# Performance work log

Measured on AMD Instinct MI355X. Metric: run time of the kernel, lower is better.

The kernel has to match this reference:

```python
import jax, jax.numpy as jnp
import numpy as np

EPS = 1e-5  # 'eps' forward arg, fixed as in typical transformer LayerNorm


def setup_inputs() -> dict:
    key = jax.random.key(0)
    ks = jax.random.split(key, 9)
    B, S, D = 4, 2048, 2048
    scale = 0.02
    return {
        "inputs": jax.random.normal(ks[0], (B, S, D), jnp.float32),
        "norm_weight": jax.random.uniform(ks[1], (D,), jnp.float32),
        "norm_bias": jax.random.normal(ks[2], (D,), jnp.float32) * scale,
        "q_weight": jax.random.normal(ks[3], (D, D), jnp.float32) * scale,
        "q_bias": jax.random.normal(ks[4], (D,), jnp.float32) * scale,
        "k_weight": jax.random.normal(ks[5], (D, D), jnp.float32) * scale,
        "k_bias": jax.random.normal(ks[6], (D,), jnp.float32) * scale,
        "v_weight": jax.random.normal(ks[7], (D, D), jnp.float32) * scale,
        "v_bias": jax.random.normal(ks[8], (D,), jnp.float32) * scale,
        "trans_b": 1,
        "shape_param": 0,
    }


def _layernorm(x, w, b, eps):
    mu = jnp.mean(x, axis=-1, keepdims=True)
    var = jnp.mean(jnp.square(x - mu), axis=-1, keepdims=True)
    return (x - mu) * jax.lax.rsqrt(var + eps) * w + b


def reference(inputs, norm_weight, norm_bias, q_weight, q_bias,
              k_weight, k_bias, v_weight, v_bias, trans_b, shape_param):
    # fused LayerNorm + Q/K/V projection (torch_mlu_ops.fused_norm_attention_project)
    normed = _layernorm(inputs, norm_weight, norm_bias, EPS)
    # trans_b==True convention: weights are [out, in] (nn.Linear layout)
    if not trans_b:
        q_weight = q_weight.T
        k_weight = None if k_weight is None else k_weight.T
        v_weight = None if v_weight is None else v_weight.T
    q = jnp.einsum('bsd,od->bso', normed, q_weight) + q_bias
    outs = [q]
    if k_weight is not None:
        outs.append(jnp.einsum('bsd,od->bso', normed, k_weight) + k_bias)
    if v_weight is not None:
        outs.append(jnp.einsum('bsd,od->bso', normed, v_weight) + v_bias)
    output = jnp.concatenate(outs, axis=-1)  # [B, S, 3*D] fused QKV
    if shape_param:
        output = output.reshape(shape_param)
    return output
```

## Files before the change

kernel.cpp:

```cpp
#include <hip/hip_runtime.h>
#include <hip/hip_bf16.h>
#include <stdint.h>

__device__ __forceinline__ uint16_t f2bf(float f) {
    union { float f; uint32_t u; } c; c.f = f;
    uint32_t u = c.u;
    return (uint16_t)((u + 0x7FFFu + ((u >> 16) & 1u)) >> 16);
}
__device__ __forceinline__ uint32_t pack2(float a, float b) {
    return (uint32_t)f2bf(a) | ((uint32_t)f2bf(b) << 16);
}

typedef __bf16 bf16x8 __attribute__((ext_vector_type(8)));
typedef float  f32x4  __attribute__((ext_vector_type(4)));

#define GLOAD_LDS16(g, l) __builtin_amdgcn_global_load_lds( \
    (const __attribute__((address_space(1))) void*)(g),     \
    (__attribute__((address_space(3))) void*)(l), 16, 0, 0)

__global__ __launch_bounds__(256) void ln_kernel(
    const float* __restrict__ x, const float* __restrict__ gw,
    const float* __restrict__ gb, uint16_t* __restrict__ y, int D)
{
    const int t = threadIdx.x;
    const size_t row = blockIdx.x;
    const float4* xr = (const float4*)(x + row * (size_t)D);
    float4 v0 = xr[2 * t], v1 = xr[2 * t + 1];

    float s  = v0.x + v0.y + v0.z + v0.w + v1.x + v1.y + v1.z + v1.w;
    float ss = v0.x * v0.x + v0.y * v0.y + v0.z * v0.z + v0.w * v0.w
             + v1.x * v1.x + v1.y * v1.y + v1.z * v1.z + v1.w * v1.w;
#pragma unroll
    for (int off = 32; off > 0; off >>= 1) {
        s  += __shfl_down(s, off);
        ss += __shfl_down(ss, off);
    }
    __shared__ float red[10];
    const int wave = t >> 6, lane = t & 63;
    if (lane == 0) { red[wave] = s; red[4 + wave] = ss; }
    __syncthreads();
    if (t == 0) {
        float S  = red[0] + red[1] + red[2] + red[3];
        float SS = red[4] + red[5] + red[6] + red[7];
        float mu = S / (float)D;
        float var = SS / (float)D - mu * mu;
        red[8] = mu;
        red[9] = rsqrtf(var + 1e-5f);
    }
    __syncthreads();
    const float mu = red[8], rstd = red[9];

    const float4* wr = (const float4*)gw;
    const float4* br = (const float4*)gb;
    float4 w0 = wr[2 * t], w1 = wr[2 * t + 1];
    float4 b0 = br[2 * t], b1 = br[2 * t + 1];

    uint4 ov;
    ov.x = pack2((v0.x - mu) * rstd * w0.x + b0.x, (v0.y - mu) * rstd * w0.y + b0.y);
    ov.y = pack2((v0.z - mu) * rstd * w0.z + b0.z, (v0.w - mu) * rstd * w0.w + b0.w);
    ov.z = pack2((v1.x - mu) * rstd * w1.x + b1.x, (v1.y - mu) * rstd * w1.y + b1.y);
    ov.w = pack2((v1.z - mu) * rstd * w1.z + b1.z, (v1.w - mu) * rstd * w1.w + b1.w);
    ((uint4*)(y + row * (size_t)D))[t] = ov;
}

__global__ __launch_bounds__(256) void wcvt_kernel(
    const float* __restrict__ wq, const float* __restrict__ wk,
    const float* __restrict__ wv, uint16_t* __restrict__ out)
{
    const size_t i = ((size_t)blockIdx.x * 256 + threadIdx.x) * 8;
    const int which = (int)(i >> 22);
    const float* src = (which == 0) ? wq : (which == 1) ? wk : wv;
    const size_t off = i & ((1u << 22) - 1);
    float4 a = *(const float4*)(src + off);
    float4 b = *(const float4*)(src + off + 4);
    uint4 ov;
    ov.x = pack2(a.x, a.y);
    ov.y = pack2(a.z, a.w);
    ov.z = pack2(b.x, b.y);
    ov.w = pack2(b.z, b.w);
    *(uint4*)(out + i) = ov;
}

__global__ __launch_bounds__(256) void qkv_gemm(
    const uint16_t* __restrict__ A, const uint16_t* __restrict__ W,
    const float* __restrict__ Bq, const float* __restrict__ Bk,
    const float* __restrict__ Bv,
    float* __restrict__ C, int M, int N, int K)
{
    __shared__ uint16_t As[128 * 32];
    __shared__ uint16_t Bs[128 * 32];

    const int t = threadIdx.x, wave = t >> 6, lane = t & 63;
    const int nb = blockIdx.x, mb = blockIdx.y;
    const int ncol0 = nb * 128;

    const int c0 = wave * 2, c1 = wave * 2 + 1;
    const int lrow = lane >> 2, lk = (lane & 3) * 8;
    const uint16_t* ga0 = A + (size_t)(mb * 128 + c0 * 16 + lrow) * K + lk;
    const uint16_t* ga1 = A + (size_t)(mb * 128 + c1 * 16 + lrow) * K + lk;
    const uint16_t* gb0 = W + (size_t)(ncol0 + c0 * 16 + lrow) * K + lk;
    const uint16_t* gb1 = W + (size_t)(ncol0 + c1 * 16 + lrow) * K + lk;
    uint16_t* la0 = &As[c0 * 512];
    uint16_t* la1 = &As[c1 * 512];
    uint16_t* lb0 = &Bs[c0 * 512];
    uint16_t* lb1 = &Bs[c1 * 512];

    f32x4 acc[4][4] = {};

    const int wm = (wave >> 1) * 64, wn = (wave & 1) * 64;
    const int fr = lane & 15, fq = (lane >> 4) * 8;

    for (int kt = 0; kt < K; kt += 32) {
        GLOAD_LDS16(ga0, la0);
        GLOAD_LDS16(ga1, la1);
        GLOAD_LDS16(gb0, lb0);
        GLOAD_LDS16(gb1, lb1);
        ga0 += 32; ga1 += 32; gb0 += 32; gb1 += 32;
        __syncthreads();

        bf16x8 af[4], bfv[4];
#pragma unroll
        for (int i = 0; i < 4; ++i)
            af[i] = *(const bf16x8*)&As[(wm + i * 16 + fr) * 32 + fq];
#pragma unroll
        for (int j = 0; j < 4; ++j)
            bfv[j] = *(const bf16x8*)&Bs[(wn + j * 16 + fr) * 32 + fq];
#pragma unroll
        for (int i = 0; i < 4; ++i)
#pragma unroll
            for (int j = 0; j < 4; ++j)
                acc[i][j] = __builtin_amdgcn_mfma_f32_16x16x32_bf16(
                    af[i], bfv[j], acc[i][j], 0, 0, 0);
        __syncthreads();
    }

    const int orow0 = mb * 128 + wm + (lane >> 4) * 4;
#pragma unroll
    for (int j = 0; j < 4; ++j) {
        const int colg = ncol0 + wn + j * 16 + fr;
        const int which = colg >> 11;
        const float* bp = (which == 0) ? Bq : (which == 1) ? Bk : Bv;
        const float bj = bp[colg & 2047];
#pragma unroll
        for (int i = 0; i < 4; ++i) {
            const int r0 = orow0 + i * 16;
#pragma unroll
            for (int r = 0; r < 4; ++r) {
                C[(size_t)(r0 + r) * N + colg] = acc[i][j][r] + bj;
            }
        }
    }
}

extern "C" void kernel_launch(void* const* d_in, const int* in_sizes, int n_in,
                              void* d_out, int out_size, void* d_ws, size_t ws_size,
                              hipStream_t stream) {
    const float* x  = (const float*)d_in[0];
    const float* nw = (const float*)d_in[1];
    const float* nb = (const float*)d_in[2];
    const float* wq = (const float*)d_in[3];
    const float* bq = (const float*)d_in[4];
    const float* wk = (const float*)d_in[5];
    const float* bk = (const float*)d_in[6];
    const float* wv = (const float*)d_in[7];
    const float* bv = (const float*)d_in[8];

    const int D = in_sizes[1];
    const int M = in_sizes[0] / D;
    const int N = 3 * D;

    uint16_t* normed = (uint16_t*)d_ws;
    uint16_t* wcat   = normed + (size_t)M * D;

    ln_kernel<<<M, 256, 0, stream>>>(x, nw, nb, normed, D);
    wcvt_kernel<<<((size_t)N * D) / (256 * 8), 256, 0, stream>>>(wq, wk, wv, wcat);
    dim3 grid(N / 128, M / 128);
    qkv_gemm<<<grid, 256, 0, stream>>>(normed, wcat, bq, bk, bv,
                                       (float*)d_out, M, N, D);
}
```

Before: 535.8 us.

## Fuse LN and weight-convert kernels, use 32x32 MFMA, group-swizzle GEMM blocks

Merges the LayerNorm and weight-conversion kernels into one launch by splitting block IDs between the two jobs, removing a kernel launch. The GEMM now uses 32x32x16 bf16 MFMA with 2x2 accumulator tiles per wave instead of 4x4 tiles of 16x16x32, cutting LDS fragment reads per MFMA. It also remaps the 1-D grid into column groups of 16 so that blocks running at the same time share B tiles, aiming for better L2 reuse. The output store pattern changes to match the 32x32 accumulator layout.

```diff
diff --git a/kernel.cpp b/kernel.cpp
--- a/kernel.cpp
+++ b/kernel.cpp
@@ -12,73 +12,74 @@
 }
 
 typedef __bf16 bf16x8 __attribute__((ext_vector_type(8)));
-typedef float  f32x4  __attribute__((ext_vector_type(4)));
+typedef float  f32x16 __attribute__((ext_vector_type(16)));
 
 #define GLOAD_LDS16(g, l) __builtin_amdgcn_global_load_lds( \
     (const __attribute__((address_space(1))) void*)(g),     \
     (__attribute__((address_space(3))) void*)(l), 16, 0, 0)
 
-__global__ __launch_bounds__(256) void ln_kernel(
+__global__ __launch_bounds__(256) void ln_wcvt(
     const float* __restrict__ x, const float* __restrict__ gw,
-    const float* __restrict__ gb, uint16_t* __restrict__ y, int D)
+    const float* __restrict__ gb, uint16_t* __restrict__ y,
+    const float* __restrict__ wq, const float* __restrict__ wk,
+    const float* __restrict__ wv, uint16_t* __restrict__ wcat,
+    int D, int M)
 {
     const int t = threadIdx.x;
-    const size_t row = blockIdx.x;
-    const float4* xr = (const float4*)(x + row * (size_t)D);
-    float4 v0 = xr[2 * t], v1 = xr[2 * t + 1];
+    if ((int)blockIdx.x < M) {
+        const size_t row = blockIdx.x;
+        const float4* xr = (const float4*)(x + row * (size_t)D);
+        float4 v0 = xr[2 * t], v1 = xr[2 * t + 1];
 
-    float s  = v0.x + v0.y + v0.z + v0.w + v1.x + v1.y + v1.z + v1.w;
-    float ss = v0.x * v0.x + v0.y * v0.y + v0.z * v0.z + v0.w * v0.w
-             + v1.x * v1.x + v1.y * v1.y + v1.z * v1.z + v1.w * v1.w;
+        float s  = v0.x + v0.y + v0.z + v0.w + v1.x + v1.y + v1.z + v1.w;
+        float ss = v0.x * v0.x + v0.y * v0.y + v0.z * v0.z + v0.w * v0.w
+                 + v1.x * v1.x + v1.y * v1.y + v1.z * v1.z + v1.w * v1.w;
 #pragma unroll
-    for (int off = 32; off > 0; off >>= 1) {
-        s  += __shfl_down(s, off);
-        ss += __shfl_down(ss, off);
+        for (int off = 32; off > 0; off >>= 1) {
+            s  += __shfl_down(s, off);
+            ss += __shfl_down(ss, off);
+        }
+        __shared__ float red[10];
+        const int wave = t >> 6, lane = t & 63;
+        if (lane == 0) { red[wave] = s; red[4 + wave] = ss; }
+        __syncthreads();
+        if (t == 0) {
+            float S  = red[0] + red[1] + red[2] + red[3];
+            float SS = red[4] + red[5] + red[6] + red[7];
+            float mu = S / (float)D;
+            float var = SS / (float)D - mu * mu;
+            red[8] = mu;
+            red[9] = rsqrtf(var + 1e-5f);
+        }
+        __syncthreads();
+        const float mu = red[8], rstd = red[9];
+
+        const float4* wr = (const float4*)gw;
+        const float4* br = (const float4*)gb;
+        float4 w0 = wr[2 * t], w1 = wr[2 * t + 1];
+        float4 b0 = br[2 * t], b1 = br[2 * t + 1];
+
+        uint4 ov;
+        ov.x = pack2((v0.x - mu) * rstd * w0.x + b0.x, (v0.y - mu) * rstd * w0.y + b0.y);
+        ov.y = pack2((v0.z - mu) * rstd * w0.z + b0.z, (v0.w - mu) * rstd * w0.w + b0.w);
+        ov.z = pack2((v1.x - mu) * rstd * w1.x + b1.x, (v1.y - mu) * rstd * w1.y + b1.y);
+        ov.w = pack2((v1.z - mu) * rstd * w1.z + b1.z, (v1.w - mu) * rstd * w1.w + b1.w);
+        ((uint4*)(y + row * (size_t)D))[t] = ov;
+    } else {
+        const size_t i = ((size_t)(blockIdx.x - M) * 256 + t) * 8;
+        const size_t per = (size_t)D * D;
+        const int which = (int)(i / per);
+        const float* src = (which == 0) ? wq : (which == 1) ? wk : wv;
+        const size_t off = i - (size_t)which * per;
+        float4 a = *(const float4*)(src + off);
+        float4 b = *(const float4*)(src + off + 4);
+        uint4 ov;
+        ov.x = pack2(a.x, a.y);
+        ov.y = pack2(a.z, a.w);
+        ov.z = pack2(b.x, b.y);
+        ov.w = pack2(b.z, b.w);
+        *(uint4*)(wcat + i) = ov;
     }
-    __shared__ float red[10];
-    const int wave = t >> 6, lane = t & 63;
-    if (lane == 0) { red[wave] = s; red[4 + wave] = ss; }
-    __syncthreads();
-    if (t == 0) {
-        float S  = red[0] + red[1] + red[2] + red[3];
-        float SS = red[4] + red[5] + red[6] + red[7];
-        float mu = S / (float)D;
-        float var = SS / (float)D - mu * mu;
-        red[8] = mu;
-        red[9] = rsqrtf(var + 1e-5f);
-    }
-    __syncthreads();
-    const float mu = red[8], rstd = red[9];
-
-    const float4* wr = (const float4*)gw;
-    const float4* br = (const float4*)gb;
-    float4 w0 = wr[2 * t], w1 = wr[2 * t + 1];
-    float4 b0 = br[2 * t], b1 = br[2 * t + 1];
-
-    uint4 ov;
-    ov.x = pack2((v0.x - mu) * rstd * w0.x + b0.x, (v0.y - mu) * rstd * w0.y + b0.y);
-    ov.y = pack2((v0.z - mu) * rstd * w0.z + b0.z, (v0.w - mu) * rstd * w0.w + b0.w);
-    ov.z = pack2((v1.x - mu) * rstd * w1.x + b1.x, (v1.y - mu) * rstd * w1.y + b1.y);
-    ov.w = pack2((v1.z - mu) * rstd * w1.z + b1.z, (v1.w - mu) * rstd * w1.w + b1.w);
-    ((uint4*)(y + row * (size_t)D))[t] = ov;
-}
-
-__global__ __launch_bounds__(256) void wcvt_kernel(
-    const float* __restrict__ wq, const float* __restrict__ wk,
-    const float* __restrict__ wv, uint16_t* __restrict__ out)
-{
-    const size_t i = ((size_t)blockIdx.x * 256 + threadIdx.x) * 8;
-    const int which = (int)(i >> 22);
-    const float* src = (which == 0) ? wq : (which == 1) ? wk : wv;
-    const size_t off = i & ((1u << 22) - 1);
-    float4 a = *(const float4*)(src + off);
-    float4 b = *(const float4*)(src + off + 4);
-    uint4 ov;
-    ov.x = pack2(a.x, a.y);
-    ov.y = pack2(a.z, a.w);
-    ov.z = pack2(b.x, b.y);
-    ov.w = pack2(b.z, b.w);
-    *(uint4*)(out + i) = ov;
 }
 
 __global__ __launch_bounds__(256) void qkv_gemm(
@@ -91,7 +92,13 @@
     __shared__ uint16_t Bs[128 * 32];
 
     const int t = threadIdx.x, wave = t >> 6, lane = t & 63;
-    const int nb = blockIdx.x, mb = blockIdx.y;
+
+    const int mbk = M >> 7;
+    const int GROUPN = 16;
+    const int bpg = GROUPN * mbk;
+    const int g = blockIdx.x / bpg, r = blockIdx.x % bpg;
+    const int nb = g * GROUPN + (r % GROUPN);
+    const int mb = r / GROUPN;
     const int ncol0 = nb * 128;
 
     const int c0 = wave * 2, c1 = wave * 2 + 1;
@@ -105,10 +112,10 @@
     uint16_t* lb0 = &Bs[c0 * 512];
     uint16_t* lb1 = &Bs[c1 * 512];
 
-    f32x4 acc[4][4] = {};
+    f32x16 acc[2][2] = {};
 
     const int wm = (wave >> 1) * 64, wn = (wave & 1) * 64;
-    const int fr = lane & 15, fq = (lane >> 4) * 8;
+    const int fm = lane & 31, fk = (lane >> 5) * 8;
 
     for (int kt = 0; kt < K; kt += 32) {
         GLOAD_LDS16(ga0, la0);
@@ -118,35 +125,34 @@
         ga0 += 32; ga1 += 32; gb0 += 32; gb1 += 32;
         __syncthreads();
 
-        bf16x8 af[4], bfv[4];
 #pragma unroll
-        for (int i = 0; i < 4; ++i)
-            af[i] = *(const bf16x8*)&As[(wm + i * 16 + fr) * 32 + fq];
-#pragma unroll
-        for (int j = 0; j < 4; ++j)
-            bfv[j] = *(const bf16x8*)&Bs[(wn + j * 16 + fr) * 32 + fq];
-#pragma unroll
-        for (int i = 0; i < 4; ++i)
-#pragma unroll
-            for (int j = 0; j < 4; ++j)
-                acc[i][j] = __builtin_amdgcn_mfma_f32_16x16x32_bf16(
-                    af[i], bfv[j], acc[i][j], 0, 0, 0);
+        for (int kk = 0; kk < 2; ++kk) {
+            bf16x8 a0 = *(const bf16x8*)&As[(wm      + fm) * 32 + kk * 16 + fk];
+            bf16x8 a1 = *(const bf16x8*)&As[(wm + 32 + fm) * 32 + kk * 16 + fk];
+            bf16x8 b0 = *(const bf16x8*)&Bs[(wn      + fm) * 32 + kk * 16 + fk];
+            bf16x8 b1 = *(const bf16x8*)&Bs[(wn + 32 + fm) * 32 + kk * 16 + fk];
+            acc[0][0] = __builtin_amdgcn_mfma_f32_32x32x16_bf16(a0, b0, acc[0][0], 0, 0, 0);
+            acc[0][1] = __builtin_amdgcn_mfma_f32_32x32x16_bf16(a0, b1, acc[0][1], 0, 0, 0);
+            acc[1][0] = __builtin_amdgcn_mfma_f32_32x32x16_bf16(a1, b0, acc[1][0], 0, 0, 0);
+            acc[1][1] = __builtin_amdgcn_mfma_f32_32x32x16_bf16(a1, b1, acc[1][1], 0, 0, 0);
+        }
         __syncthreads();
     }
 
-    const int orow0 = mb * 128 + wm + (lane >> 4) * 4;
+    const int rq = 4 * (lane >> 5);
 #pragma unroll
-    for (int j = 0; j < 4; ++j) {
-        const int colg = ncol0 + wn + j * 16 + fr;
-        const int which = colg >> 11;
+    for (int ni = 0; ni < 2; ++ni) {
+        const int colg = ncol0 + wn + ni * 32 + fm;
+        const int which = (colg >= 2 * K) ? 2 : (colg >= K ? 1 : 0);
         const float* bp = (which == 0) ? Bq : (which == 1) ? Bk : Bv;
-        const float bj = bp[colg & 2047];
+        const float bj = bp[colg - which * K];
 #pragma unroll
-        for (int i = 0; i < 4; ++i) {
-            const int r0 = orow0 + i * 16;
+        for (int mi = 0; mi < 2; ++mi) {
+            const int rbase = mb * 128 + wm + mi * 32 + rq;
 #pragma unroll
-            for (int r = 0; r < 4; ++r) {
-                C[(size_t)(r0 + r) * N + colg] = acc[i][j][r] + bj;
+            for (int reg = 0; reg < 16; ++reg) {
+                const int row = rbase + (reg & 3) + 8 * (reg >> 2);
+                C[(size_t)row * N + colg] = acc[mi][ni][reg] + bj;
             }
         }
     }
@@ -172,9 +178,10 @@
     uint16_t* normed = (uint16_t*)d_ws;
     uint16_t* wcat   = normed + (size_t)M * D;
 
-    ln_kernel<<<M, 256, 0, stream>>>(x, nw, nb, normed, D);
-    wcvt_kernel<<<((size_t)N * D) / (256 * 8), 256, 0, stream>>>(wq, wk, wv, wcat);
-    dim3 grid(N / 128, M / 128);
-    qkv_gemm<<<grid, 256, 0, stream>>>(normed, wcat, bq, bk, bv,
-                                       (float*)d_out, M, N, D);
+    const int wcvt_blocks = (int)(((size_t)N * D) / (256 * 8));
+    ln_wcvt<<<M + wcvt_blocks, 256, 0, stream>>>(x, nw, nb, normed,
+                                                 wq, wk, wv, wcat, D, M);
+    const int nblocks = (M / 128) * (N / 128);
+    qkv_gemm<<<nblocks, 256, 0, stream>>>(normed, wcat, bq, bk, bv,
+                                          (float*)d_out, M, N, D);
 }
```

After: 583.9 us. 1.09x slower.
